# Optimization experiments

Measured on AMD Instinct MI355X. Metric: run time of the kernel, lower is better.

The kernel has to match this reference:

```python
import jax, jax.numpy as jnp
import numpy as np

N_START, N_TO, E, H = 100000, 50000, 1000000, 128

def setup_inputs() -> dict:
    key = jax.random.key(0)
    ks = jax.random.split(key, 8)
    return {
        "z_start": jax.random.normal(ks[0], (N_START, H), dtype=jnp.float32),
        "z_to": jax.random.normal(ks[1], (N_TO, H), dtype=jnp.float32),
        "row": jax.random.randint(ks[2], (E,), 0, N_START, dtype=jnp.int64),
        "col": jax.random.randint(ks[3], (E,), 0, N_TO, dtype=jnp.int64),
        "W1": jax.random.normal(ks[4], (2 * H, H), dtype=jnp.float32) * (1.0 / np.sqrt(2 * H)),
        "b1": jnp.zeros((H,), dtype=jnp.float32),
        "W2": jax.random.normal(ks[5], (H, 1), dtype=jnp.float32) * (1.0 / np.sqrt(H)),
        "b2": jnp.zeros((1,), dtype=jnp.float32),
    }

def reference(z_start, z_to, row, col, W1, b1, W2, b2):
    # gather node embeddings by edge endpoints, concat along feature dim
    z = jnp.concatenate([z_start[row], z_to[col]], axis=-1)  # [E, 2H]
    h = jax.nn.relu(z @ W1 + b1)                              # [E, H]
    out = h @ W2 + b2                                         # [E, 1]
    return out.reshape(-1)
```

## Files before the change

### kernel.cpp

```cpp
#include <hip/hip_runtime.h>
#include <hip/hip_bf16.h>
#include <stdint.h>

typedef unsigned short u16;
typedef unsigned long long u64;
typedef __attribute__((ext_vector_type(8))) short short8;
typedef __attribute__((ext_vector_type(4))) float float4v;

__device__ __forceinline__ u16 f2bf(float x) {
    union { float f; unsigned int u; } v; v.f = x;
    unsigned int r = v.u + 0x7fffu + ((v.u >> 16) & 1u);
    return (u16)(r >> 16);
}

__device__ __forceinline__ void ld_g2l16(const void* g, void* l) {
    __builtin_amdgcn_global_load_lds(
        (const __attribute__((address_space(1))) void*)g,
        (__attribute__((address_space(3))) void*)l, 16, 0, 0);
}

__device__ __forceinline__ float sbyte_f(int w, int j) {
    return (float)((w << (24 - 8 * j)) >> 24);
}

__global__ __launch_bounds__(256) void w1_pack(
    const float* __restrict__ W1, u16* __restrict__ w1p, int* __restrict__ cursor)
{
    if (blockIdx.x == 0 && threadIdx.x < 8) cursor[threadIdx.x] = 0;
    int w = blockIdx.x * 256 + threadIdx.x;
    int lanep = w & 63, t = (w >> 6) & 7, kc = w >> 9;
    short8 o;
#pragma unroll
    for (int j = 0; j < 8; ++j) {
        int k = kc * 32 + (lanep >> 4) * 8 + j;
        int n = t * 16 + (lanep & 15);
        o[j] = (short)f2bf(W1[k * 128 + n]);
    }
    *(short8*)(w1p + (size_t)w * 8) = o;
}

__global__ __launch_bounds__(256) void uv_gemm(
    const float* __restrict__ zs, const float* __restrict__ zt,
    const u16* __restrict__ w1p, const float* __restrict__ b1,
    char* __restrict__ U8, char* __restrict__ V8,
    float* __restrict__ su, float* __restrict__ sv,
    int M1, int M2, int nU)
{
    __shared__ u16 Alds[16384];
    __shared__ u16 Blds[16384];

    const int tid = threadIdx.x, wave = tid >> 6, lane = tid & 63;
    const int m15 = lane & 15, quad = lane >> 4;
    const bool isV = (int)blockIdx.x >= nU;
    const float* zsrc = isV ? zt : zs;
    char* dst = isV ? V8 : U8;
    float* sdst = isV ? sv : su;
    const int row0 = (isV ? ((int)blockIdx.x - nU) : (int)blockIdx.x) * 128;
    const int M = isV ? M2 : M1;
    const int nrows = (M - row0) < 128 ? (M - row0) : 128;

    const u16* wsrc = w1p + (isV ? 16384 : 0);
#pragma unroll
    for (int it = 0; it < 8; ++it) {
        int off = (wave * 8 + it) * 1024;
        ld_g2l16((const char*)wsrc + off + lane * 16, (char*)Blds + off);
    }

#pragma unroll
    for (int it = 0; it < 8; ++it) {
        int r = it * 16 + wave * 4 + (lane >> 4);
        int q = lane & 15;
        int c = q ^ (r & 15);
        int rr = r < nrows ? r : (nrows - 1);
        const float4* src = (const float4*)(zsrc + (size_t)(row0 + rr) * 128 + c * 8);
        float4 x = src[0], y = src[1];
        short8 o;
        o[0] = (short)f2bf(x.x); o[1] = (short)f2bf(x.y);
        o[2] = (short)f2bf(x.z); o[3] = (short)f2bf(x.w);
        o[4] = (short)f2bf(y.x); o[5] = (short)f2bf(y.y);
        o[6] = (short)f2bf(y.z); o[7] = (short)f2bf(y.w);
        *(short8*)((char*)Alds + r * 256 + q * 16) = o;
    }

    __builtin_amdgcn_s_waitcnt(0);
    __syncthreads();

    float4v acc[2][8];
#pragma unroll
    for (int a = 0; a < 2; ++a)
#pragma unroll
        for (int b = 0; b < 8; ++b)
            acc[a][b] = (float4v){0.f, 0.f, 0.f, 0.f};

#pragma unroll
    for (int kc = 0; kc < 4; ++kc) {
        short8 Af[2];
#pragma unroll
        for (int mtl = 0; mtl < 2; ++mtl) {
            int r = wave * 32 + mtl * 16 + m15;
            int c = kc * 4 + quad;
            int q = c ^ (r & 15);
            Af[mtl] = *(const short8*)((const char*)Alds + r * 256 + q * 16);
        }
#pragma unroll
        for (int t = 0; t < 8; ++t) {
            short8 Bf = *(const short8*)((const char*)Blds + (kc * 8 + t) * 1024 + lane * 16);
#pragma unroll
            for (int mtl = 0; mtl < 2; ++mtl)
                acc[mtl][t] = __builtin_amdgcn_mfma_f32_16x16x32_bf16(
                    Af[mtl], Bf, acc[mtl][t], 0, 0, 0);
        }
    }

    float b1v[8];
#pragma unroll
    for (int t = 0; t < 8; ++t) b1v[t] = isV ? 0.f : b1[t * 16 + m15];

#pragma unroll
    for (int mtl = 0; mtl < 2; ++mtl) {
#pragma unroll
        for (int r = 0; r < 4; ++r) {
            const int rr = wave * 32 + mtl * 16 + quad * 4 + r;
            float vals[8];
            float vmax = 0.f;
#pragma unroll
            for (int t = 0; t < 8; ++t) {
                float x = acc[mtl][t][r] + b1v[t];
                vals[t] = x;
                vmax = fmaxf(vmax, fabsf(x));
            }
            vmax = fmaxf(vmax, __shfl_xor(vmax, 1));
            vmax = fmaxf(vmax, __shfl_xor(vmax, 2));
            vmax = fmaxf(vmax, __shfl_xor(vmax, 4));
            vmax = fmaxf(vmax, __shfl_xor(vmax, 8));
            const float scl = vmax * (1.f / 127.f);
            const float rs = vmax > 0.f ? 127.f / vmax : 0.f;
            if (rr < nrows) {
                if (m15 == 0) sdst[row0 + rr] = scl;
#pragma unroll
                for (int t = 0; t < 8; ++t) {
                    int q = __float2int_rn(vals[t] * rs);
                    q = q > 127 ? 127 : (q < -127 ? -127 : q);
                    dst[(size_t)(row0 + rr) * 128 + t * 16 + m15] = (char)q;
                }
            }
        }
    }
}

__global__ __launch_bounds__(256) void edge_bin(
    const int* __restrict__ row, const int* __restrict__ col,
    u64* __restrict__ tup, int* __restrict__ cursor,
    int E, float binv, int C,
    const char* __restrict__ U8, const char* __restrict__ V8,
    const float* __restrict__ su, const float* __restrict__ sv,
    const float* __restrict__ W2, const float* __restrict__ b2,
    float* __restrict__ out)
{
    __shared__ int lcnt[8];
    __shared__ int lbase[8];
    const int tid = threadIdx.x;
    if (tid < 8) lcnt[tid] = 0;
    __syncthreads();
    const int eb = blockIdx.x * 4096;
    int rr[16], cc[16], bb[16], rk[16];
#pragma unroll
    for (int it = 0; it < 16; ++it) {
        int e = eb + it * 256 + tid;
        rk[it] = -1;
        if (e < E) {
            int r = row[e], c = col[e];
            int b = (int)((float)r * binv);
            b = b > 7 ? 7 : b;
            rr[it] = r; cc[it] = c; bb[it] = b;
            rk[it] = atomicAdd(&lcnt[b], 1);
        }
    }
    __syncthreads();
    if (tid < 8) lbase[tid] = atomicAdd(&cursor[tid], lcnt[tid]);
    __syncthreads();
#pragma unroll
    for (int it = 0; it < 16; ++it) {
        if (rk[it] < 0) continue;
        int e = eb + it * 256 + tid;
        int slot = lbase[bb[it]] + rk[it];
        if (slot < C) {
            tup[(size_t)bb[it] * C + slot] =
                (u64)(unsigned)rr[it] | ((u64)(unsigned)cc[it] << 17) | ((u64)(unsigned)e << 34);
        } else {
            float a = su[rr[it]], bs = sv[cc[it]];
            const signed char* up = (const signed char*)(U8 + (size_t)rr[it] * 128);
            const signed char* vp = (const signed char*)(V8 + (size_t)cc[it] * 128);
            float s = 0.f;
            for (int j = 0; j < 128; ++j) {
                float h = fmaf(a, (float)up[j], bs * (float)vp[j]);
                h = fmaxf(h, 0.f);
                s = fmaf(h, W2[j], s);
            }
            out[e] = s + b2[0];
        }
    }
}

__global__ __launch_bounds__(256) void edge_out(
    const char* __restrict__ U8, const char* __restrict__ V8,
    const float* __restrict__ su, const float* __restrict__ sv,
    const u64* __restrict__ tup, const int* __restrict__ cursor,
    const float* __restrict__ W2, const float* __restrict__ b2,
    float* __restrict__ out, int C, int chunks_per_bin)
{
    const int tid = threadIdx.x, m15 = tid & 15, g = tid >> 4;
    const int bin = (int)blockIdx.x & 7;
    int chunk = (int)blockIdx.x >> 3;
    int cnt = cursor[bin];
    cnt = cnt < C ? cnt : C;
    float w2f[8];
#pragma unroll
    for (int j = 0; j < 8; ++j) w2f[j] = W2[m15 * 8 + j];
    const float b2v = b2[0];
    const u64* tb = tup + (size_t)bin * C;

    for (; chunk * 128 < cnt; chunk += chunks_per_bin) {
        const int base = chunk * 128;

        u64 t[8];
#pragma unroll
        for (int it = 0; it < 8; ++it) {
            int idx = base + it * 16 + g;
            t[it] = tb[idx < cnt ? idx : cnt - 1];
        }
        __builtin_amdgcn_sched_barrier(0);

        uint2 qu[8], qv[8];
        float fsu[8], fsv[8];
#pragma unroll
        for (int it = 0; it < 8; ++it) {
            int r = (int)(t[it] & 0x1FFFF);
            int c = (int)((t[it] >> 17) & 0x1FFFF);
            qu[it] = *(const uint2*)(U8 + (size_t)(unsigned)r * 128 + m15 * 8);
            qv[it] = *(const uint2*)(V8 + (size_t)(unsigned)c * 128 + m15 * 8);
            fsu[it] = su[r];
            fsv[it] = sv[c];
        }
        __builtin_amdgcn_sched_barrier(0);

#pragma unroll
        for (int it = 0; it < 8; ++it) {
            const float a = fsu[it], b = fsv[it];
            const int u0 = (int)qu[it].x, u1 = (int)qu[it].y;
            const int v0 = (int)qv[it].x, v1 = (int)qv[it].y;
            float s = 0.f;
#pragma unroll
            for (int j = 0; j < 4; ++j) {
                float h0 = fmaf(a, sbyte_f(u0, j), b * sbyte_f(v0, j));
                h0 = fmaxf(h0, 0.f);
                s = fmaf(h0, w2f[j], s);
                float h1 = fmaf(a, sbyte_f(u1, j), b * sbyte_f(v1, j));
                h1 = fmaxf(h1, 0.f);
                s = fmaf(h1, w2f[4 + j], s);
            }
            s += __shfl_xor(s, 1);
            s += __shfl_xor(s, 2);
            s += __shfl_xor(s, 4);
            s += __shfl_xor(s, 8);
            int idx = base + it * 16 + g;
            if (m15 == 0 && idx < cnt) out[(int)(t[it] >> 34)] = s + b2v;
        }
    }
}

__global__ __launch_bounds__(256) void edge_mlp_naive(
    const float* __restrict__ zs, const float* __restrict__ zt,
    const int* __restrict__ row, const int* __restrict__ col,
    const float* __restrict__ W1, const float* __restrict__ b1,
    const float* __restrict__ W2, const float* __restrict__ b2,
    float* __restrict__ out, int E)
{
    __shared__ float zr[4][256];
    int wave = threadIdx.x >> 6, lane = threadIdx.x & 63;
    int e = blockIdx.x * 4 + wave;
    int ec = e < E ? e : E - 1;
    const float* a = zs + (size_t)row[ec] * 128;
    const float* bb = zt + (size_t)col[ec] * 128;
    zr[wave][lane] = a[lane];
    zr[wave][64 + lane] = a[64 + lane];
    zr[wave][128 + lane] = bb[lane];
    zr[wave][192 + lane] = bb[64 + lane];
    __syncthreads();
    float h0 = b1[lane], h1 = b1[64 + lane];
    for (int k = 0; k < 256; ++k) {
        float zk = zr[wave][k];
        h0 = fmaf(zk, W1[k * 128 + lane], h0);
        h1 = fmaf(zk, W1[k * 128 + 64 + lane], h1);
    }
    h0 = h0 > 0.f ? h0 : 0.f;
    h1 = h1 > 0.f ? h1 : 0.f;
    float s = fmaf(h0, W2[lane], h1 * W2[64 + lane]);
    for (int m = 1; m < 64; m <<= 1) s += __shfl_xor(s, m);
    if (lane == 0 && e < E) out[e] = s + b2[0];
}

extern "C" void kernel_launch(void* const* d_in, const int* in_sizes, int n_in,
                              void* d_out, int out_size, void* d_ws, size_t ws_size,
                              hipStream_t stream) {
    const float* zs = (const float*)d_in[0];
    const float* zt = (const float*)d_in[1];
    const int*  row = (const int*)d_in[2];
    const int*  col = (const int*)d_in[3];
    const float* W1 = (const float*)d_in[4];
    const float* b1 = (const float*)d_in[5];
    const float* W2 = (const float*)d_in[6];
    const float* b2 = (const float*)d_in[7];
    float* out = (float*)d_out;

    const int nzs = in_sizes[0];
    const int nzt = in_sizes[1];
    const int E   = in_sizes[2];
    const int M1  = nzs / 128;
    const int M2  = nzt / 128;

    int C = 65536;
    while (C < E / 4 + 1024) C <<= 1;

    const size_t tup_b = (size_t)8 * C * 8;
    const size_t need = tup_b + 64 + (size_t)M1 * 4 + (size_t)M2 * 4 + 65536
                      + (size_t)nzs + (size_t)nzt;
    const bool shapes_ok = (M1 <= 131072) && (M2 <= 131072) && (E > 0) && (E < (1 << 30));

    if (!shapes_ok || ws_size < need) {
        int nb = (E + 3) / 4;
        edge_mlp_naive<<<nb, 256, 0, stream>>>(zs, zt, row, col, W1, b1, W2, b2, out, E);
        return;
    }

    u64* tup    = (u64*)d_ws;
    int* cursor = (int*)((char*)d_ws + tup_b);
    float* su   = (float*)((char*)cursor + 64);
    float* sv   = su + M1;
    u16* w1p    = (u16*)(sv + M2);
    char* U8    = (char*)(w1p + 32768);
    char* V8    = U8 + (size_t)nzs;

    w1_pack<<<16, 256, 0, stream>>>(W1, w1p, cursor);

    const int nU = (M1 + 127) / 128;
    const int nV = (M2 + 127) / 128;
    uv_gemm<<<nU + nV, 256, 0, stream>>>(zs, zt, w1p, b1, U8, V8, su, sv, M1, M2, nU);

    const int rpb = (M1 + 7) / 8;
    const float binv = 1.0f / (float)rpb;
    edge_bin<<<(E + 4095) / 4096, 256, 0, stream>>>(
        row, col, tup, cursor, E, binv, C, U8, V8, su, sv, W2, b2, out);

    const int cpb = 1024;
    edge_out<<<8 * cpb, 256, 0, stream>>>(U8, V8, su, sv, tup, cursor, W2, b2, out, C, cpb);
}
```

Before: 179.5 us.

## Use packed fp16 dot math in edge_out and drop LDS staging in uv_gemm

edge_out now gives each edge 8 lanes instead of 16, and each lane loads 16 bytes. The int8 values are decoded with a magic-number bias into packed fp16, then the relu and the W2 dot product run through fdot2. The grid is halved to match. uv_gemm no longer stages A and B through LDS: each wave loads its A rows straight into registers, reads W1 fragments from global memory, and declares an occupancy hint. Together these cut ALU work per edge and LDS traffic, at the cost of fp16 rounding of the hidden activations and repeated global reads of W1.

```diff
diff --git a/kernel.cpp b/kernel.cpp
--- a/kernel.cpp
+++ b/kernel.cpp
@@ -6,6 +6,7 @@
 typedef unsigned long long u64;
 typedef __attribute__((ext_vector_type(8))) short short8;
 typedef __attribute__((ext_vector_type(4))) float float4v;
+typedef __attribute__((ext_vector_type(2))) _Float16 v2h;
 
 __device__ __forceinline__ u16 f2bf(float x) {
     union { float f; unsigned int u; } v; v.f = x;
@@ -13,14 +14,16 @@
     return (u16)(r >> 16);
 }
 
-__device__ __forceinline__ void ld_g2l16(const void* g, void* l) {
-    __builtin_amdgcn_global_load_lds(
-        (const __attribute__((address_space(1))) void*)g,
-        (__attribute__((address_space(3))) void*)l, 16, 0, 0);
-}
-
-__device__ __forceinline__ float sbyte_f(int w, int j) {
-    return (float)((w << (24 - 8 * j)) >> 24);
+__device__ __forceinline__ v2h mk2h(unsigned int u) {
+    union { unsigned int u; v2h h; } c; c.u = u; return c.h;
+}
+
+__device__ __forceinline__ float dot2acc(v2h a, v2h b, float s) {
+#if __has_builtin(__builtin_amdgcn_fdot2)
+    return __builtin_amdgcn_fdot2(a, b, s, false);
+#else
+    return fmaf((float)a[0], (float)b[0], fmaf((float)a[1], (float)b[1], s));
+#endif
 }
 
 __global__ __launch_bounds__(256) void w1_pack(
@@ -39,16 +42,13 @@
     *(short8*)(w1p + (size_t)w * 8) = o;
 }
 
-__global__ __launch_bounds__(256) void uv_gemm(
+__global__ __launch_bounds__(256, 3) void uv_gemm(
     const float* __restrict__ zs, const float* __restrict__ zt,
     const u16* __restrict__ w1p, const float* __restrict__ b1,
     char* __restrict__ U8, char* __restrict__ V8,
     float* __restrict__ su, float* __restrict__ sv,
     int M1, int M2, int nU)
 {
-    __shared__ u16 Alds[16384];
-    __shared__ u16 Blds[16384];
-
     const int tid = threadIdx.x, wave = tid >> 6, lane = tid & 63;
     const int m15 = lane & 15, quad = lane >> 4;
     const bool isV = (int)blockIdx.x >= nU;
@@ -58,32 +58,33 @@
     const int row0 = (isV ? ((int)blockIdx.x - nU) : (int)blockIdx.x) * 128;
     const int M = isV ? M2 : M1;
     const int nrows = (M - row0) < 128 ? (M - row0) : 128;
-
-    const u16* wsrc = w1p + (isV ? 16384 : 0);
-#pragma unroll
-    for (int it = 0; it < 8; ++it) {
-        int off = (wave * 8 + it) * 1024;
-        ld_g2l16((const char*)wsrc + off + lane * 16, (char*)Blds + off);
-    }
-
-#pragma unroll
-    for (int it = 0; it < 8; ++it) {
-        int r = it * 16 + wave * 4 + (lane >> 4);
-        int q = lane & 15;
-        int c = q ^ (r & 15);
+    const char* wsrc = (const char*)(w1p + (isV ? 16384 : 0));
+
+    float4 afl[2][4][2];
+#pragma unroll
+    for (int mtl = 0; mtl < 2; ++mtl) {
+        int r = wave * 32 + mtl * 16 + m15;
         int rr = r < nrows ? r : (nrows - 1);
-        const float4* src = (const float4*)(zsrc + (size_t)(row0 + rr) * 128 + c * 8);
-        float4 x = src[0], y = src[1];
-        short8 o;
-        o[0] = (short)f2bf(x.x); o[1] = (short)f2bf(x.y);
-        o[2] = (short)f2bf(x.z); o[3] = (short)f2bf(x.w);
-        o[4] = (short)f2bf(y.x); o[5] = (short)f2bf(y.y);
-        o[6] = (short)f2bf(y.z); o[7] = (short)f2bf(y.w);
-        *(short8*)((char*)Alds + r * 256 + q * 16) = o;
-    }
-
-    __builtin_amdgcn_s_waitcnt(0);
-    __syncthreads();
+        const float* rowp = zsrc + (size_t)(row0 + rr) * 128 + quad * 8;
+#pragma unroll
+        for (int kc = 0; kc < 4; ++kc) {
+            afl[mtl][kc][0] = *(const float4*)(rowp + kc * 32);
+            afl[mtl][kc][1] = *(const float4*)(rowp + kc * 32 + 4);
+        }
+    }
+    short8 Af[2][4];
+#pragma unroll
+    for (int mtl = 0; mtl < 2; ++mtl)
+#pragma unroll
+        for (int kc = 0; kc < 4; ++kc) {
+            float4 x = afl[mtl][kc][0], y = afl[mtl][kc][1];
+            short8 o;
+            o[0] = (short)f2bf(x.x); o[1] = (short)f2bf(x.y);
+            o[2] = (short)f2bf(x.z); o[3] = (short)f2bf(x.w);
+            o[4] = (short)f2bf(y.x); o[5] = (short)f2bf(y.y);
+            o[6] = (short)f2bf(y.z); o[7] = (short)f2bf(y.w);
+            Af[mtl][kc] = o;
+        }
 
     float4v acc[2][8];
 #pragma unroll
@@ -94,22 +95,16 @@
 
 #pragma unroll
     for (int kc = 0; kc < 4; ++kc) {
-        short8 Af[2];
-#pragma unroll
-        for (int mtl = 0; mtl < 2; ++mtl) {
-            int r = wave * 32 + mtl * 16 + m15;
-            int c = kc * 4 + quad;
-            int q = c ^ (r & 15);
-            Af[mtl] = *(const short8*)((const char*)Alds + r * 256 + q * 16);
-        }
-#pragma unroll
-        for (int t = 0; t < 8; ++t) {
-            short8 Bf = *(const short8*)((const char*)Blds + (kc * 8 + t) * 1024 + lane * 16);
+        short8 Bf[8];
+#pragma unroll
+        for (int t = 0; t < 8; ++t)
+            Bf[t] = *(const short8*)(wsrc + ((kc * 8 + t) * 1024 + lane * 16));
+#pragma unroll
+        for (int t = 0; t < 8; ++t)
 #pragma unroll
             for (int mtl = 0; mtl < 2; ++mtl)
                 acc[mtl][t] = __builtin_amdgcn_mfma_f32_16x16x32_bf16(
-                    Af[mtl], Bf, acc[mtl][t], 0, 0, 0);
-        }
+                    Af[mtl][kc], Bf[t], acc[mtl][t], 0, 0, 0);
     }
 
     float b1v[8];
@@ -209,36 +204,44 @@
     const float* __restrict__ W2, const float* __restrict__ b2,
     float* __restrict__ out, int C, int chunks_per_bin)
 {
-    const int tid = threadIdx.x, m15 = tid & 15, g = tid >> 4;
+    const int tid = threadIdx.x, m7 = tid & 7, g = tid >> 3;
     const int bin = (int)blockIdx.x & 7;
     int chunk = (int)blockIdx.x >> 3;
     int cnt = cursor[bin];
     cnt = cnt < C ? cnt : C;
-    float w2f[8];
-#pragma unroll
-    for (int j = 0; j < 8; ++j) w2f[j] = W2[m15 * 8 + j];
+
+    v2h w2e[4], w2o[4];
+#pragma unroll
+    for (int w = 0; w < 4; ++w) {
+        int base = m7 * 16 + w * 4;
+        w2e[w] = (v2h){(_Float16)W2[base + 0], (_Float16)W2[base + 2]};
+        w2o[w] = (v2h){(_Float16)W2[base + 1], (_Float16)W2[base + 3]};
+    }
     const float b2v = b2[0];
+    const v2h zero2 = (v2h){(_Float16)0.f, (_Float16)0.f};
+    const _Float16 mh = (_Float16)(-1152.f);
+    const v2h m1152 = (v2h){mh, mh};
     const u64* tb = tup + (size_t)bin * C;
 
-    for (; chunk * 128 < cnt; chunk += chunks_per_bin) {
-        const int base = chunk * 128;
+    for (; chunk * 256 < cnt; chunk += chunks_per_bin) {
+        const int base = chunk * 256;
 
         u64 t[8];
 #pragma unroll
         for (int it = 0; it < 8; ++it) {
-            int idx = base + it * 16 + g;
+            int idx = base + it * 32 + g;
             t[it] = tb[idx < cnt ? idx : cnt - 1];
         }
         __builtin_amdgcn_sched_barrier(0);
 
-        uint2 qu[8], qv[8];
+        uint4 qu[8], qv[8];
         float fsu[8], fsv[8];
 #pragma unroll
         for (int it = 0; it < 8; ++it) {
             int r = (int)(t[it] & 0x1FFFF);
             int c = (int)((t[it] >> 17) & 0x1FFFF);
-            qu[it] = *(const uint2*)(U8 + (size_t)(unsigned)r * 128 + m15 * 8);
-            qv[it] = *(const uint2*)(V8 + (size_t)(unsigned)c * 128 + m15 * 8);
+            qu[it] = *(const uint4*)(U8 + (size_t)(unsigned)r * 128 + m7 * 16);
+            qv[it] = *(const uint4*)(V8 + (size_t)(unsigned)c * 128 + m7 * 16);
             fsu[it] = su[r];
             fsv[it] = sv[c];
         }
@@ -247,24 +250,31 @@
 #pragma unroll
         for (int it = 0; it < 8; ++it) {
             const float a = fsu[it], b = fsv[it];
-            const int u0 = (int)qu[it].x, u1 = (int)qu[it].y;
-            const int v0 = (int)qv[it].x, v1 = (int)qv[it].y;
+            const _Float16 ah = (_Float16)a, bh = (_Float16)b;
+            const v2h a2 = (v2h){ah, ah}, bb2 = (v2h){bh, bh};
+            const unsigned int* uw = (const unsigned int*)&qu[it];
+            const unsigned int* vw = (const unsigned int*)&qv[it];
             float s = 0.f;
 #pragma unroll
-            for (int j = 0; j < 4; ++j) {
-                float h0 = fmaf(a, sbyte_f(u0, j), b * sbyte_f(v0, j));
-                h0 = fmaxf(h0, 0.f);
-                s = fmaf(h0, w2f[j], s);
-                float h1 = fmaf(a, sbyte_f(u1, j), b * sbyte_f(v1, j));
-                h1 = fmaxf(h1, 0.f);
-                s = fmaf(h1, w2f[4 + j], s);
+            for (int w = 0; w < 4; ++w) {
+                unsigned int xu = uw[w] ^ 0x80808080u;
+                unsigned int xv = vw[w] ^ 0x80808080u;
+                v2h due = mk2h((xu & 0x00FF00FFu) | 0x64006400u) + m1152;
+                v2h duo = mk2h(((xu >> 8) & 0x00FF00FFu) | 0x64006400u) + m1152;
+                v2h dve = mk2h((xv & 0x00FF00FFu) | 0x64006400u) + m1152;
+                v2h dvo = mk2h(((xv >> 8) & 0x00FF00FFu) | 0x64006400u) + m1152;
+                v2h he = __builtin_elementwise_fma(a2, due, bb2 * dve);
+                he = __builtin_elementwise_max(he, zero2);
+                s = dot2acc(he, w2e[w], s);
+                v2h ho = __builtin_elementwise_fma(a2, duo, bb2 * dvo);
+                ho = __builtin_elementwise_max(ho, zero2);
+                s = dot2acc(ho, w2o[w], s);
             }
             s += __shfl_xor(s, 1);
             s += __shfl_xor(s, 2);
             s += __shfl_xor(s, 4);
-            s += __shfl_xor(s, 8);
-            int idx = base + it * 16 + g;
-            if (m15 == 0 && idx < cnt) out[(int)(t[it] >> 34)] = s + b2v;
+            int idx = base + it * 32 + g;
+            if (m7 == 0 && idx < cnt) out[(int)(t[it] >> 34)] = s + b2v;
         }
     }
 }
@@ -352,6 +362,6 @@
     edge_bin<<<(E + 4095) / 4096, 256, 0, stream>>>(
         row, col, tup, cursor, E, binv, C, U8, V8, su, sv, W2, b2, out);
 
-    const int cpb = 1024;
+    const int cpb = 512;
     edge_out<<<8 * cpb, 256, 0, stream>>>(U8, V8, su, sv, tup, cursor, W2, b2, out, C, cpb);
 }
```

Result: slower. 184.7 us (+2.9%).
